# Optimization experiments

Measured on AMD Instinct MI355X. Metric: run time of the kernel, lower is better.

Reference implementation:

```python
import jax, jax.numpy as jnp
import numpy as np

DIM = 1024
H_MID = max(8, DIM // 2)   # 512
H_LOW = max(8, DIM // 4)   # 256


def setup_inputs() -> dict:
    key = jax.random.key(0)
    ks = jax.random.split(key, 10)
    s = lambda fan_in: 1.0 / np.sqrt(fan_in)
    x = jax.random.normal(ks[0], (4, 8192, DIM), dtype=jnp.float32)
    return {
        "x": x,
        "gamma": jnp.ones((DIM,), jnp.float32),
        "beta": jnp.zeros((DIM,), jnp.float32),
        "W1": jax.random.uniform(ks[1], (DIM, H_MID), jnp.float32, -s(DIM), s(DIM)),
        "b1": jax.random.uniform(ks[2], (H_MID,), jnp.float32, -s(DIM), s(DIM)),
        "W2": jax.random.uniform(ks[3], (H_MID, H_MID), jnp.float32, -s(H_MID), s(H_MID)),
        "b2": jax.random.uniform(ks[4], (H_MID,), jnp.float32, -s(H_MID), s(H_MID)),
        "W3": jax.random.uniform(ks[5], (H_MID, H_LOW), jnp.float32, -s(H_MID), s(H_MID)),
        "b3": jax.random.uniform(ks[6], (H_LOW,), jnp.float32, -s(H_MID), s(H_MID)),
        "W4": jax.random.uniform(ks[7], (H_LOW, DIM), jnp.float32, -s(H_LOW), s(H_LOW)),
        "b4": jax.random.uniform(ks[8], (DIM,), jnp.float32, -s(H_LOW), s(H_LOW)),
    }


def _layernorm(x, gamma, beta, eps=1e-5):
    mu = jnp.mean(x, axis=-1, keepdims=True)
    var = jnp.mean(jnp.square(x - mu), axis=-1, keepdims=True)
    return (x - mu) * jax.lax.rsqrt(var + eps) * gamma + beta


def reference(x, gamma, beta, W1, b1, W2, b2, W3, b3, W4, b4):
    gelu = lambda h: jax.nn.gelu(h, approximate=False)  # torch default: exact erf GELU
    h = _layernorm(x, gamma, beta)                      # (B,S,D)
    h = gelu(jnp.einsum("bsd,dm->bsm", h, W1) + b1)    # (B,S,D/2)
    h = gelu(jnp.einsum("bsm,mn->bsn", h, W2) + b2)    # (B,S,D/2)
    h = gelu(jnp.einsum("bsn,nl->bsl", h, W3) + b3)    # (B,S,D/4)
    h = jnp.einsum("bsl,ld->bsd", h, W4) + b4          # (B,S,D)
    return x + h
```

## Files before the change

### kernel.cpp

```cpp
#include <hip/hip_runtime.h>


typedef short short8 __attribute__((ext_vector_type(8)));
typedef float floatx4 __attribute__((ext_vector_type(4)));
typedef unsigned short ushort4v __attribute__((ext_vector_type(4)));
typedef unsigned int uint2v __attribute__((ext_vector_type(2)));

__device__ __forceinline__ unsigned short f2bf(float f) {
    union { float f; unsigned int u; } a; a.f = f;
    unsigned int u = a.u;
    return (unsigned short)((u + 0x7FFFu + ((u >> 16) & 1u)) >> 16);
}

__device__ __forceinline__ float bf2f(unsigned short h) {
    union { unsigned int u; float f; } a; a.u = ((unsigned int)h) << 16;
    return a.f;
}

__device__ __forceinline__ unsigned int pkbf(float a, float b) {
    return (unsigned int)f2bf(a) | ((unsigned int)f2bf(b) << 16);
}

__device__ __forceinline__ float gelu_fast(float v) {
    float u = 0.7978845608f * v * (1.0f + 0.044715f * v * v);
    float e = __builtin_amdgcn_exp2f(u * 2.885390082f);
    float t = 1.0f - 2.0f * __builtin_amdgcn_rcpf(1.0f + e);
    return 0.5f * v * (1.0f + t);
}

__device__ __forceinline__ void gl_lds16(const unsigned short* g, unsigned short* l) {
    __builtin_amdgcn_global_load_lds(
        (const __attribute__((address_space(1))) void*)g,
        (__attribute__((address_space(3))) void*)l, 16, 0, 0);
}

__global__ __launch_bounds__(256) void conv_all_kernel(
    const float* __restrict__ W1, const float* __restrict__ W2,
    const float* __restrict__ W3, const float* __restrict__ W4,
    const float* __restrict__ gamma,
    unsigned short* __restrict__ Wt1, unsigned short* __restrict__ Wt2,
    unsigned short* __restrict__ Wt3, unsigned short* __restrict__ Wt4) {
    int b = blockIdx.x;
    const float* W; unsigned short* Wt; int K, N; const float* sc = nullptr;
    if (b < 2048)      { W = W1; Wt = Wt1; K = 1024; N = 512;  sc = gamma; }
    else if (b < 3072) { W = W2; Wt = Wt2; K = 512;  N = 512;  b -= 2048; }
    else if (b < 3584) { W = W3; Wt = Wt3; K = 512;  N = 256;  b -= 3072; }
    else               { W = W4; Wt = Wt4; K = 256;  N = 1024; b -= 3584; }
    int t = b * 256 + threadIdx.x;
    int sh = 31 - __clz(N);
    int k = t >> sh, n = t & (N - 1);
    float v = W[t];
    if (sc) v *= sc[k];
    Wt[(size_t)n * K + k] = f2bf(v);
}

__global__ __launch_bounds__(256) void u1c1_init_kernel(
    const float* __restrict__ b1, float* __restrict__ u1, float* __restrict__ c1,
    int N) {
    int n = blockIdx.x * 256 + threadIdx.x;
    if (n >= N) return;
    u1[n] = 0.f;
    c1[n] = b1[n];
}

__global__ __launch_bounds__(256) void u1c1_kernel(
    const float* __restrict__ W1, const float* __restrict__ gamma,
    const float* __restrict__ beta, float* __restrict__ u1,
    float* __restrict__ c1) {
    const int N = 512;
    __shared__ float gs[16], bs[16];
    int n = threadIdx.x;
    int k0 = blockIdx.x * 16;
    if (n < 16) { gs[n] = gamma[k0 + n]; bs[n] = beta[k0 + n]; }
    __syncthreads();
    float ua = 0.f, ca = 0.f, ub = 0.f, cb = 0.f;
#pragma unroll
    for (int i = 0; i < 16; i++) {
        float w0 = W1[(size_t)(k0 + i) * N + n];
        float w1 = W1[(size_t)(k0 + i) * N + n + 256];
        ua += gs[i] * w0; ca += bs[i] * w0;
        ub += gs[i] * w1; cb += bs[i] * w1;
    }
    atomicAdd(&u1[n], ua);       atomicAdd(&c1[n], ca);
    atomicAdd(&u1[n + 256], ub); atomicAdd(&c1[n + 256], cb);
}

__global__ __launch_bounds__(256) void ln_stats_kernel(
    const float* __restrict__ x, float* __restrict__ mu, float* __restrict__ rs,
    unsigned short* __restrict__ xb) {
    const int D = 1024;
    int row = blockIdx.x * 4 + (threadIdx.x >> 6);
    int lane = threadIdx.x & 63;
    const float4* xr = (const float4*)(x + (size_t)row * D);
    float s = 0.f, ss = 0.f;
#pragma unroll
    for (int i = 0; i < 4; i++) {
        float4 v = xr[lane + 64 * i];
        s  += v.x + v.y + v.z + v.w;
        ss += v.x * v.x + v.y * v.y + v.z * v.z + v.w * v.w;
        if (xb) {
            ushort4v o;
            o.x = f2bf(v.x); o.y = f2bf(v.y); o.z = f2bf(v.z); o.w = f2bf(v.w);
            *(ushort4v*)(xb + (size_t)row * D + 4 * (lane + 64 * i)) = o;
        }
    }
#pragma unroll
    for (int off = 32; off; off >>= 1) {
        s  += __shfl_xor(s, off);
        ss += __shfl_xor(ss, off);
    }
    if (lane == 0) {
        float m = s * (1.0f / 1024.0f);
        mu[row] = m;
        rs[row] = rsqrtf(ss * (1.0f / 1024.0f) - m * m + 1e-5f);
    }
}

template <int EPMODE, bool AF32, int NBN, int NT, int KT>
__global__ __launch_bounds__(256) void gemm_kernel(
    const void* __restrict__ Aptr, const unsigned short* __restrict__ Bt,
    void* __restrict__ Out,
    const float* __restrict__ bias,
    const float* __restrict__ u1,
    const float* __restrict__ mu,
    const float* __restrict__ rs,
    const void* __restrict__ resid)
{
    constexpr int BM = 128, BN = 128, BK = 64;
    constexpr int N = NT, K = KT;
    __shared__ unsigned short As[BM][BK];
    __shared__ unsigned short Bs[BN][BK];

    const int tid  = threadIdx.x;
    const int wave = tid >> 6;
    const int lane = tid & 63;
    const int q    = lane >> 4;
    const int l16  = lane & 15;
    const int wm   = wave & 1;
    const int wn   = wave >> 1;

    const int id   = blockIdx.x;
    const int xcd  = id & 7;
    const int slot = id >> 3;
    const int m0   = (xcd + 8 * (slot / NBN)) * BM;
    const int n0   = (slot % NBN) * BN;

    const int sr  = tid >> 3;
    const int sc  = tid & 7;
    const int sg  = sc ^ (sr & 7);
    unsigned short* lA = &As[0][0] + (wave << 9);
    unsigned short* lB = &Bs[0][0] + (wave << 9);
    const unsigned short* gb0 = Bt + (size_t)(n0 + sr) * K + sg * 8;
    const unsigned short* ga0 = nullptr;
    if (!AF32) ga0 = (const unsigned short*)Aptr + (size_t)(m0 + sr) * K + sg * 8;

    floatx4 acc[4][4] = {};

#pragma unroll
    for (int k0 = 0; k0 < K; k0 += BK) {
        if (AF32) {
            const float* A = (const float*)Aptr;
            int c = tid & 15, r0 = tid >> 4;
#pragma unroll
            for (int i = 0; i < 8; i++) {
                int r = r0 + 16 * i;
                float4 v = *(const float4*)(A + (size_t)(m0 + r) * K + k0 + c * 4);
                ushort4v o;
                o.x = f2bf(v.x); o.y = f2bf(v.y);
                o.z = f2bf(v.z); o.w = f2bf(v.w);
                int idx = r * 64 + (((c >> 1) ^ (r & 7)) << 3) + ((c & 1) << 2);
                *(ushort4v*)(&As[0][0] + idx) = o;
            }
        } else {
#pragma unroll
            for (int c = 0; c < 4; c++)
                gl_lds16(ga0 + k0 + (size_t)(32 * c) * K, lA + c * 2048);
        }
#pragma unroll
        for (int c = 0; c < 4; c++)
            gl_lds16(gb0 + k0 + (size_t)(32 * c) * K, lB + c * 2048);
        __syncthreads();

#pragma unroll
        for (int kk = 0; kk < 2; kk++) {
            const int gsw = ((kk * 4 + q) ^ (l16 & 7)) * 8;
            short8 a[4], b[4];
#pragma unroll
            for (int mt = 0; mt < 4; mt++)
                a[mt] = *(const short8*)(&As[0][0] + (wm * 64 + mt * 16 + l16) * 64 + gsw);
#pragma unroll
            for (int nt = 0; nt < 4; nt++)
                b[nt] = *(const short8*)(&Bs[0][0] + (wn * 64 + nt * 16 + l16) * 64 + gsw);
#pragma unroll
            for (int nt = 0; nt < 4; nt++)
#pragma unroll
                for (int mt = 0; mt < 4; mt++)
                    acc[nt][mt] = __builtin_amdgcn_mfma_f32_16x16x32_bf16(
                        b[nt], a[mt], acc[nt][mt], 0, 0, 0);
        }
        __syncthreads();
    }

    float rs4[4], mu4[4];
    if constexpr (EPMODE == 0) {
#pragma unroll
        for (int mt = 0; mt < 4; mt++) {
            const int row = m0 + wm * 64 + mt * 16 + l16;
            rs4[mt] = rs[row];
            mu4[mt] = mu[row];
        }
    }
#pragma unroll
    for (int nt = 0; nt < 4; nt++) {
        const int nbase = n0 + wn * 64 + nt * 16 + q * 4;
        const float4 bv = *(const float4*)(bias + nbase);
        float4 uv = {0.f, 0.f, 0.f, 0.f};
        if constexpr (EPMODE == 0) uv = *(const float4*)(u1 + nbase);
#pragma unroll
        for (int mt = 0; mt < 4; mt++) {
            const int row = m0 + wm * 64 + mt * 16 + l16;
            const size_t off = (size_t)row * N + nbase;
            float v0 = acc[nt][mt][0], v1 = acc[nt][mt][1];
            float v2 = acc[nt][mt][2], v3 = acc[nt][mt][3];
            if constexpr (EPMODE == 0) {
                v0 = gelu_fast(rs4[mt] * (v0 - mu4[mt] * uv.x) + bv.x);
                v1 = gelu_fast(rs4[mt] * (v1 - mu4[mt] * uv.y) + bv.y);
                v2 = gelu_fast(rs4[mt] * (v2 - mu4[mt] * uv.z) + bv.z);
                v3 = gelu_fast(rs4[mt] * (v3 - mu4[mt] * uv.w) + bv.w);
                uint2v o; o.x = pkbf(v0, v1); o.y = pkbf(v2, v3);
                *(uint2v*)((unsigned short*)Out + off) = o;
            } else if constexpr (EPMODE == 1) {
                v0 = gelu_fast(v0 + bv.x);
                v1 = gelu_fast(v1 + bv.y);
                v2 = gelu_fast(v2 + bv.z);
                v3 = gelu_fast(v3 + bv.w);
                uint2v o; o.x = pkbf(v0, v1); o.y = pkbf(v2, v3);
                *(uint2v*)((unsigned short*)Out + off) = o;
            } else if constexpr (EPMODE == 2) {
                const float4 rv = *(const float4*)((const float*)resid + off);
                float4 o;
                o.x = v0 + bv.x + rv.x;
                o.y = v1 + bv.y + rv.y;
                o.z = v2 + bv.z + rv.z;
                o.w = v3 + bv.w + rv.w;
                *(float4*)((float*)Out + off) = o;
            } else {
                const ushort4v rv =
                    *(const ushort4v*)((const unsigned short*)resid + off);
                float4 o;
                o.x = v0 + bv.x + bf2f(rv.x);
                o.y = v1 + bv.y + bf2f(rv.y);
                o.z = v2 + bv.z + bf2f(rv.z);
                o.w = v3 + bv.w + bf2f(rv.w);
                *(float4*)((float*)Out + off) = o;
            }
        }
    }
}

extern "C" void kernel_launch(void* const* d_in, const int* in_sizes, int n_in,
                              void* d_out, int out_size, void* d_ws, size_t ws_size,
                              hipStream_t stream) {
    const float* x     = (const float*)d_in[0];
    const float* gamma = (const float*)d_in[1];
    const float* beta  = (const float*)d_in[2];
    const float* W1    = (const float*)d_in[3];
    const float* b1    = (const float*)d_in[4];
    const float* W2    = (const float*)d_in[5];
    const float* b2    = (const float*)d_in[6];
    const float* W3    = (const float*)d_in[7];
    const float* b3    = (const float*)d_in[8];
    const float* W4    = (const float*)d_in[9];
    const float* b4    = (const float*)d_in[10];
    float* out = (float*)d_out;

    const int D = 1024, H1 = 512, H2 = 512;
    const int M = in_sizes[0] / D;

    char* ws = (char*)d_ws;
    unsigned short* Wt1 = (unsigned short*)(ws + 0);
    unsigned short* Wt2 = (unsigned short*)(ws + 1048576);
    unsigned short* Wt3 = (unsigned short*)(ws + 1572864);
    unsigned short* Wt4 = (unsigned short*)(ws + 1835008);
    float* u1           = (float*)(ws + 2359296);
    float* c1           = (float*)(ws + 2361344);
    float* muv          = (float*)(ws + 2363392);
    float* rsv          = (float*)(ws + 2494464);
    unsigned short* h1  = (unsigned short*)(ws + 2625536);
    unsigned short* h2  = (unsigned short*)(ws + 36179968);
    unsigned short* h3  = h1;
    size_t base_end     = 36179968 + (size_t)M * H2 * 2;
    unsigned short* xb  = (unsigned short*)(ws + base_end);
    bool use_xb = (ws_size >= base_end + (size_t)M * D * 2);

    const int NBM = M / 128;

    conv_all_kernel<<<4608, 256, 0, stream>>>(W1, W2, W3, W4, gamma,
                                              Wt1, Wt2, Wt3, Wt4);
    u1c1_init_kernel<<<(H1 + 255) / 256, 256, 0, stream>>>(b1, u1, c1, H1);
    u1c1_kernel<<<D / 16, 256, 0, stream>>>(W1, gamma, beta, u1, c1);

    ln_stats_kernel<<<M / 4, 256, 0, stream>>>(x, muv, rsv, use_xb ? xb : nullptr);

    if (use_xb) {
        gemm_kernel<0, false, 4, 512, 1024><<<4 * NBM, 256, 0, stream>>>(
            xb, Wt1, h1, c1, u1, muv, rsv, nullptr);
    } else {
        gemm_kernel<0, true, 4, 512, 1024><<<4 * NBM, 256, 0, stream>>>(
            x,  Wt1, h1, c1, u1, muv, rsv, nullptr);
    }
    gemm_kernel<1, false, 4, 512, 512><<<4 * NBM, 256, 0, stream>>>(
        h1, Wt2, h2, b2, nullptr, nullptr, nullptr, nullptr);
    gemm_kernel<1, false, 2, 256, 512><<<2 * NBM, 256, 0, stream>>>(
        h2, Wt3, h3, b3, nullptr, nullptr, nullptr, nullptr);
    if (use_xb) {
        gemm_kernel<3, false, 8, 1024, 256><<<8 * NBM, 256, 0, stream>>>(
            h3, Wt4, out, b4, nullptr, nullptr, nullptr, xb);
    } else {
        gemm_kernel<2, false, 8, 1024, 256><<<8 * NBM, 256, 0, stream>>>(
            h3, Wt4, out, b4, nullptr, nullptr, nullptr, x);
    }
}
```

Measured before the change: 404.3 us.

## Add 256x256-tile double-buffered GEMM kernel for first two layers

Adds a new 512-thread GEMM kernel with 256x256 output tiles, LDS double buffering through direct global-to-LDS loads, explicit vmcnt waits and barriers, and MFMA priority hints. It is used for the first two layers (LN-fused W1 and W2) in place of the 128x128 kernel. The aim is more data reuse per LDS load and overlap of global prefetch with MFMA work. The cost is much higher register and LDS pressure, plus fewer blocks per layer.

```diff
diff --git a/kernel.cpp b/kernel.cpp
--- a/kernel.cpp
+++ b/kernel.cpp
@@ -33,6 +33,10 @@
         (const __attribute__((address_space(1))) void*)g,
         (__attribute__((address_space(3))) void*)l, 16, 0, 0);
 }
+
+#define BARX() asm volatile("s_barrier" ::: "memory")
+#define VMW4() asm volatile("s_waitcnt vmcnt(4)" ::: "memory")
+#define VMW0() asm volatile("s_waitcnt vmcnt(0)" ::: "memory")
 
 __global__ __launch_bounds__(256) void conv_all_kernel(
     const float* __restrict__ W1, const float* __restrict__ W2,
@@ -116,7 +120,185 @@
     }
 }
 
-template <int EPMODE, bool AF32, int NBN, int NT, int KT>
+__device__ __forceinline__ void ldA8(const unsigned short* base, short8 (&a)[8]) {
+#pragma unroll
+    for (int mt = 0; mt < 8; mt++) a[mt] = *(const short8*)(base + mt * 512);
+}
+__device__ __forceinline__ void ldB2(const unsigned short* base, short8 (&bb)[2]) {
+    bb[0] = *(const short8*)(base);
+    bb[1] = *(const short8*)(base + 512);
+}
+template <int CH>
+__device__ __forceinline__ void mm16(const short8 (&a)[8], const short8 (&bb)[2],
+                                     floatx4 (&acc)[8][4]) {
+    __builtin_amdgcn_s_setprio(1);
+#pragma unroll
+    for (int mt = 0; mt < 8; mt++)
+#pragma unroll
+        for (int nt = 0; nt < 2; nt++)
+            acc[mt][CH * 2 + nt] = __builtin_amdgcn_mfma_f32_16x16x32_bf16(
+                bb[nt], a[mt], acc[mt][CH * 2 + nt], 0, 0, 0);
+    __builtin_amdgcn_s_setprio(0);
+}
+
+template <int KLEN, bool PF>
+__device__ __forceinline__ void do_tile(
+    const unsigned short* aK0, const unsigned short* aK1,
+    const unsigned short* bK0, const unsigned short* bK1,
+    unsigned short* stA0, unsigned short* stA1,
+    unsigned short* stB0, unsigned short* stB1,
+    const unsigned short* gAs, const unsigned short* gBs,
+    short8 (&a)[8], short8 (&bb)[2], floatx4 (&acc)[8][4]) {
+    ldA8(aK0, a);
+    ldB2(bK0, bb);
+    if (PF) {
+        gl_lds16(gAs, stA0);
+        gl_lds16(gAs + (size_t)128 * KLEN, stA0 + 4096);
+    }
+    mm16<0>(a, bb, acc);
+    BARX();
+    ldB2(bK0 + 1024, bb);
+    if (PF) {
+        gl_lds16(gBs, stB0);
+        gl_lds16(gBs + (size_t)128 * KLEN, stB0 + 4096);
+    }
+    mm16<1>(a, bb, acc);
+    if (PF) { VMW4(); } else { VMW0(); }
+    BARX();
+    ldA8(aK1, a);
+    ldB2(bK1, bb);
+    if (PF) {
+        gl_lds16(gAs + 32, stA1);
+        gl_lds16(gAs + 32 + (size_t)128 * KLEN, stA1 + 4096);
+    }
+    mm16<0>(a, bb, acc);
+    BARX();
+    ldB2(bK1 + 1024, bb);
+    if (PF) {
+        gl_lds16(gBs + 32, stB1);
+        gl_lds16(gBs + 32 + (size_t)128 * KLEN, stB1 + 4096);
+    }
+    mm16<1>(a, bb, acc);
+    if (PF) { VMW4(); }
+    BARX();
+}
+
+template <int EPMODE, int NBN, int NT, int NOUT, int KLEN>
+__global__ __launch_bounds__(512, 2) void gemm256_kernel(
+    const unsigned short* __restrict__ A, const unsigned short* __restrict__ Bt,
+    unsigned short* __restrict__ Out,
+    const float* __restrict__ bias,
+    const float* __restrict__ u1,
+    const float* __restrict__ mu,
+    const float* __restrict__ rs)
+{
+    __shared__ unsigned short lds[2][2][2][8192];
+
+    const int tid  = threadIdx.x;
+    const int wave = tid >> 6;
+    const int lane = tid & 63;
+    const int q    = lane >> 4;
+    const int l16  = lane & 15;
+    const int wm   = wave >> 2;
+    const int wn   = wave & 3;
+
+    const int id   = blockIdx.x;
+    const int xcd  = id & 7;
+    const int slot = id >> 3;
+    const int m0   = (xcd + 8 * (slot / NBN)) * 256;
+    const int n0   = (slot % NBN) * 256;
+
+    const unsigned short* gAs = A  + (size_t)(m0 + (tid >> 2)) * KLEN + (tid & 3) * 8;
+    const unsigned short* gBs = Bt + (size_t)(n0 + (tid >> 2)) * KLEN + (tid & 3) * 8;
+
+    const int wo = wave << 9;
+    unsigned short* stA00 = &lds[0][0][0][0] + wo;
+    unsigned short* stA01 = &lds[0][0][1][0] + wo;
+    unsigned short* stB00 = &lds[0][1][0][0] + wo;
+    unsigned short* stB01 = &lds[0][1][1][0] + wo;
+    unsigned short* stA10 = &lds[1][0][0][0] + wo;
+    unsigned short* stA11 = &lds[1][0][1][0] + wo;
+    unsigned short* stB10 = &lds[1][1][0][0] + wo;
+    unsigned short* stB11 = &lds[1][1][1][0] + wo;
+
+    const int aoff = (wm * 128 + l16) * 32 + q * 8;
+    const int boff = (wn * 64 + l16) * 32 + q * 8;
+    const unsigned short* aF00 = &lds[0][0][0][0] + aoff;
+    const unsigned short* aF01 = &lds[0][0][1][0] + aoff;
+    const unsigned short* bF00 = &lds[0][1][0][0] + boff;
+    const unsigned short* bF01 = &lds[0][1][1][0] + boff;
+    const unsigned short* aF10 = &lds[1][0][0][0] + aoff;
+    const unsigned short* aF11 = &lds[1][0][1][0] + aoff;
+    const unsigned short* bF10 = &lds[1][1][0][0] + boff;
+    const unsigned short* bF11 = &lds[1][1][1][0] + boff;
+
+    floatx4 acc[8][4] = {};
+    short8 a[8], bb[2];
+
+    gl_lds16(gAs,                           stA00);
+    gl_lds16(gAs + (size_t)128 * KLEN,      stA00 + 4096);
+    gl_lds16(gBs,                           stB00);
+    gl_lds16(gBs + (size_t)128 * KLEN,      stB00 + 4096);
+    gl_lds16(gAs + 32,                      stA01);
+    gl_lds16(gAs + 32 + (size_t)128 * KLEN, stA01 + 4096);
+    gl_lds16(gBs + 32,                      stB01);
+    gl_lds16(gBs + 32 + (size_t)128 * KLEN, stB01 + 4096);
+    VMW4();
+    BARX();
+    gAs += 64; gBs += 64;
+
+    for (int t = 0; t + 2 < NT; t += 2) {
+        do_tile<KLEN, true>(aF00, aF01, bF00, bF01, stA10, stA11, stB10, stB11,
+                            gAs, gBs, a, bb, acc);
+        gAs += 64; gBs += 64;
+        do_tile<KLEN, true>(aF10, aF11, bF10, bF11, stA00, stA01, stB00, stB01,
+                            gAs, gBs, a, bb, acc);
+        gAs += 64; gBs += 64;
+    }
+    do_tile<KLEN, true>(aF00, aF01, bF00, bF01, stA10, stA11, stB10, stB11,
+                        gAs, gBs, a, bb, acc);
+    do_tile<KLEN, false>(aF10, aF11, bF10, bF11, stA00, stA01, stB00, stB01,
+                         gAs, gBs, a, bb, acc);
+
+    float rs8[8], mu8[8];
+    if constexpr (EPMODE == 0) {
+#pragma unroll
+        for (int ma = 0; ma < 8; ma++) {
+            const int row = m0 + wm * 128 + ma * 16 + l16;
+            rs8[ma] = rs[row];
+            mu8[ma] = mu[row];
+        }
+    }
+#pragma unroll
+    for (int na = 0; na < 4; na++) {
+        const int nb = n0 + wn * 64 + na * 16 + q * 4;
+        const float4 bv = *(const float4*)(bias + nb);
+        float4 uv = {0.f, 0.f, 0.f, 0.f};
+        if constexpr (EPMODE == 0) uv = *(const float4*)(u1 + nb);
+#pragma unroll
+        for (int ma = 0; ma < 8; ma++) {
+            const int row = m0 + wm * 128 + ma * 16 + l16;
+            const size_t off = (size_t)row * NOUT + nb;
+            float v0 = acc[ma][na][0], v1 = acc[ma][na][1];
+            float v2 = acc[ma][na][2], v3 = acc[ma][na][3];
+            if constexpr (EPMODE == 0) {
+                v0 = gelu_fast(rs8[ma] * (v0 - mu8[ma] * uv.x) + bv.x);
+                v1 = gelu_fast(rs8[ma] * (v1 - mu8[ma] * uv.y) + bv.y);
+                v2 = gelu_fast(rs8[ma] * (v2 - mu8[ma] * uv.z) + bv.z);
+                v3 = gelu_fast(rs8[ma] * (v3 - mu8[ma] * uv.w) + bv.w);
+            } else {
+                v0 = gelu_fast(v0 + bv.x);
+                v1 = gelu_fast(v1 + bv.y);
+                v2 = gelu_fast(v2 + bv.z);
+                v3 = gelu_fast(v3 + bv.w);
+            }
+            uint2v o; o.x = pkbf(v0, v1); o.y = pkbf(v2, v3);
+            *(uint2v*)(Out + off) = o;
+        }
+    }
+}
+
+template <int EPMODE, bool AF32, int NBN, int NT_, int KT>
 __global__ __launch_bounds__(256) void gemm_kernel(
     const void* __restrict__ Aptr, const unsigned short* __restrict__ Bt,
     void* __restrict__ Out,
@@ -127,7 +309,7 @@
     const void* __restrict__ resid)
 {
     constexpr int BM = 128, BN = 128, BK = 64;
-    constexpr int N = NT, K = KT;
+    constexpr int N = NT_, K = KT;
     __shared__ unsigned short As[BM][BK];
     __shared__ unsigned short Bs[BN][BK];
 
@@ -303,14 +485,14 @@
     ln_stats_kernel<<<M / 4, 256, 0, stream>>>(x, muv, rsv, use_xb ? xb : nullptr);
 
     if (use_xb) {
-        gemm_kernel<0, false, 4, 512, 1024><<<4 * NBM, 256, 0, stream>>>(
-            xb, Wt1, h1, c1, u1, muv, rsv, nullptr);
+        gemm256_kernel<0, 2, 16, 512, 1024><<<(M / 256) * 2, 512, 0, stream>>>(
+            xb, Wt1, h1, c1, u1, muv, rsv);
     } else {
         gemm_kernel<0, true, 4, 512, 1024><<<4 * NBM, 256, 0, stream>>>(
-            x,  Wt1, h1, c1, u1, muv, rsv, nullptr);
-    }
-    gemm_kernel<1, false, 4, 512, 512><<<4 * NBM, 256, 0, stream>>>(
-        h1, Wt2, h2, b2, nullptr, nullptr, nullptr, nullptr);
+            x, Wt1, h1, c1, u1, muv, rsv, nullptr);
+    }
+    gemm256_kernel<1, 2, 8, 512, 512><<<(M / 256) * 2, 512, 0, stream>>>(
+        h1, Wt2, h2, b2, nullptr, nullptr, nullptr);
     gemm_kernel<1, false, 2, 256, 512><<<2 * NBM, 256, 0, stream>>>(
         h2, Wt3, h3, b3, nullptr, nullptr, nullptr, nullptr);
     if (use_xb) {
```

Measured after the change: 398.3 us. About the same (-1.5%).
